# Optimization experiments

Hardware: AMD Instinct MI355X
Metric: run time of the kernel (lower is better)

The kernel has to match this reference:

```python
import jax, jax.numpy as jnp
import numpy as np

B, T, C, H = 2, 2048, 1024, 16  # batch, seq, n_embd, n_head


def setup_inputs() -> dict:
    key = jax.random.key(0)
    k1, k2, k3 = jax.random.split(key, 3)
    scale = 0.02
    return {
        "x": jax.random.normal(k1, (B, T, C), dtype=jnp.float32),
        "W_attn": jax.random.normal(k2, (3 * C, C), dtype=jnp.float32) * scale,
        "b_attn": jnp.zeros((3 * C,), dtype=jnp.float32),
        "W_proj": jax.random.normal(k3, (C, C), dtype=jnp.float32) * scale,
        "b_proj": jnp.zeros((C,), dtype=jnp.float32),
        "alpha": jnp.asarray(1.0, dtype=jnp.float32),
        "beta": jnp.asarray(0.1, dtype=jnp.float32),
        "gamma": jnp.asarray(0.1, dtype=jnp.float32),
    }


def reference(x, W_attn, b_attn, W_proj, b_proj, alpha, beta, gamma):
    Bx, Tx, Cx = x.shape
    d = Cx // H  # head dim
    qkv = x @ W_attn.T + b_attn                      # [B,T,3C]
    q, k, v = jnp.split(qkv, 3, axis=-1)

    def to_heads(t):
        return t.reshape(Bx, Tx, H, d).transpose(0, 2, 1, 3)  # [B,H,T,d]

    q, k, v = to_heads(q), to_heads(k), to_heads(v)

    inv_sqrt_d = jnp.asarray(1.0 / np.sqrt(d), dtype=x.dtype)
    scores = jnp.einsum('bhtd,bhsd->bhts', q, k) * inv_sqrt_d  # [B,H,T,T]

    causal = jnp.tril(jnp.ones((Tx, Tx), dtype=bool))
    scores = jnp.where(causal, scores, -jnp.inf)
    att = jax.nn.softmax(scores, axis=-1)

    # Id buffer = softmax(10000*eye) == identity; MC buffer = softmax(10000*tril)
    # == uniform causal prefix average: MC[i, j<=i] = 1/(i+1).
    id_m = jnp.eye(Tx, dtype=x.dtype)
    mc = causal.astype(x.dtype) / jnp.arange(1, Tx + 1, dtype=x.dtype)[:, None]

    shaped = beta * att + alpha * id_m - gamma * mc  # dropout p=0 -> identity
    y = jnp.einsum('bhts,bhsd->bhtd', shaped, v)     # [B,H,T,d]
    y = y.transpose(0, 2, 1, 3).reshape(Bx, Tx, Cx)
    return y @ W_proj.T + b_proj
```

## Files before the change

### kernel.cpp

```cpp
#include <hip/hip_runtime.h>
#include <stdint.h>

#define Bsz  2
#define Tseq 2048
#define Cemb 1024
#define NH   16
#define HD   64

typedef __attribute__((ext_vector_type(8))) __bf16 bf16x8;
typedef __attribute__((ext_vector_type(4))) float  f32x4;
typedef __attribute__((ext_vector_type(8))) unsigned short u16x8;

#define MFMA16(a, b, c) __builtin_amdgcn_mfma_f32_16x16x32_bf16((a), (b), (c), 0, 0, 0)

__device__ __forceinline__ unsigned short f2bf(float f) {
  union { float f; unsigned int u; } v; v.f = f;
  unsigned int u = v.u;
  u += 0x7fffu + ((u >> 16) & 1u);
  return (unsigned short)(u >> 16);
}
__device__ __forceinline__ float bf2f(unsigned short h) {
  union { unsigned int u; float f; } v; v.u = ((unsigned int)h) << 16;
  return v.f;
}
__device__ __forceinline__ unsigned int pack_bf2(float a, float b) {
  union { float f; unsigned int u; } va, vb; va.f = a; vb.f = b;
  return __builtin_amdgcn_perm(vb.u + 0x8000u, va.u + 0x8000u, 0x07060302u);
}

typedef __attribute__((address_space(1))) const unsigned int GU;
typedef __attribute__((address_space(3))) unsigned int LU;
__device__ __forceinline__ void load_lds16(const void* g, void* l) {
  __builtin_amdgcn_global_load_lds((GU*)g, (LU*)l, 16, 0, 0);
}

#define XE  4194304
#define WAE 3145728
__global__ void cast3_kernel(const float* __restrict__ x,
                             const float* __restrict__ wa,
                             const float* __restrict__ wp,
                             unsigned short* __restrict__ out) {
  const int i = (blockIdx.x * blockDim.x + threadIdx.x) * 4;
  const float* src;
  int off;
  if (i < XE) { src = x; off = i; }
  else if (i < XE + WAE) { src = wa; off = i - XE; }
  else { src = wp; off = i - (XE + WAE); }
  const float4 f = *(const float4*)(src + off);
  ushort4 o;
  o.x = f2bf(f.x); o.y = f2bf(f.y); o.z = f2bf(f.z); o.w = f2bf(f.w);
  *(ushort4*)(out + i) = o;
}

__global__ __launch_bounds__(256) void gemm_qkv_kernel(
    const unsigned short* __restrict__ A,
    const unsigned short* __restrict__ Bw,
    const float* __restrict__ bias,
    unsigned short* __restrict__ qkv,
    unsigned short* __restrict__ vt) {
  const int K = Cemb;
  __shared__ unsigned short sA[128 * 32];
  __shared__ unsigned short sB[128 * 32];
  const int tid = threadIdx.x;
  const int wave = tid >> 6, lane = tid & 63;
  const int quad = lane >> 4, lrow = lane & 15;
  const int l7 = lrow & 7;
  const int wm = (wave >> 1) * 64, wn = (wave & 1) * 64;
  const int tileM = blockIdx.y * 128, tileN = blockIdx.x * 128;

  f32x4 acc[4][4];
#pragma unroll
  for (int i = 0; i < 4; ++i)
#pragma unroll
    for (int j = 0; j < 4; ++j) acc[i][j] = (f32x4){0.f, 0.f, 0.f, 0.f};

  for (int k0 = 0; k0 < K; k0 += 32) {
    __syncthreads();
#pragma unroll
    for (int s = 0; s < 2; ++s) {
      const int cid = tid + s * 256;
      const int r = cid >> 2, ko = (cid & 3) * 8;
      load_lds16(&A[(size_t)(tileM + r) * K + k0 + ko], &sA[cid * 8]);
      load_lds16(&Bw[(size_t)(tileN + r) * K + k0 + ko], &sB[cid * 8]);
    }
    __syncthreads();
    bf16x8 af[4], bfm[4];
#pragma unroll
    for (int mt = 0; mt < 4; ++mt)
      af[mt] = *(const bf16x8*)&sA[(wm + mt * 16 + lrow) * 32 + quad * 8];
#pragma unroll
    for (int nt = 0; nt < 4; ++nt)
      bfm[nt] = *(const bf16x8*)&sB[(wn + nt * 16 + lrow) * 32 + quad * 8];
#pragma unroll
    for (int mt = 0; mt < 4; ++mt)
#pragma unroll
      for (int nt = 0; nt < 4; ++nt)
        acc[mt][nt] = MFMA16(af[mt], bfm[nt], acc[mt][nt]);
  }

  __syncthreads();
  unsigned short* sEp = sA + wave * 1024;
  float bias_v[4];
#pragma unroll
  for (int nt = 0; nt < 4; ++nt) bias_v[nt] = bias[tileN + wn + nt * 16 + lrow];
  const int gn0 = tileN + wn;
  const int part = gn0 >> 10, h = (gn0 & 1023) >> 6;
  const float qscl = (part == 0) ? 0.125f : 1.0f;

#pragma unroll
  for (int mt = 0; mt < 4; ++mt) {
#pragma unroll
    for (int nt = 0; nt < 4; ++nt)
#pragma unroll
      for (int reg = 0; reg < 4; ++reg) {
        const int q = quad * 4 + reg;
        const int ch = (nt * 2 + (lrow >> 3)) ^ (q & 7);
        sEp[q * 64 + ch * 8 + l7] = f2bf((acc[mt][nt][reg] + bias_v[nt]) * qscl);
      }
    __builtin_amdgcn_wave_barrier();
#pragma unroll
    for (int i = 0; i < 2; ++i) {
      const int c = i * 64 + lane;
      const int r = c >> 3, ch2 = c & 7;
      const u16x8 row = *(const u16x8*)&sEp[r * 64 + ((ch2 ^ (r & 7)) << 3)];
      const int gm = tileM + wm + mt * 16 + r;
      const int bb = gm >> 11, t = gm & 2047;
      *(u16x8*)&qkv[((((size_t)part * Bsz + bb) * NH + h) * Tseq + t) * HD + ch2 * 8] = row;
    }
    if (part == 2) {
      unsigned int w[8];
#pragma unroll
      for (int q = 0; q < 16; q += 2) {
        const unsigned short a0 =
            sEp[q * 64 + (((lane >> 3) ^ (q & 7)) << 3) + (lane & 7)];
        const unsigned short a1 =
            sEp[(q + 1) * 64 + (((lane >> 3) ^ ((q + 1) & 7)) << 3) + (lane & 7)];
        w[q >> 1] = (unsigned int)a0 | ((unsigned int)a1 << 16);
      }
      const int gm0 = tileM + wm + mt * 16;
      const int bb = gm0 >> 11, t0 = gm0 & 2047;
      unsigned short* dst = &vt[(((size_t)bb * NH + h) * HD + lane) * Tseq + t0];
      *(uint4*)(dst) = *(const uint4*)&w[0];
      *(uint4*)(dst + 8) = *(const uint4*)&w[4];
    }
    __builtin_amdgcn_wave_barrier();
  }
}

__global__ __launch_bounds__(256) void gemm_proj_kernel(
    const unsigned short* __restrict__ A,
    const unsigned short* __restrict__ Bw,
    const float* __restrict__ bias,
    float* __restrict__ out) {
  const int K = Cemb;
  __shared__ unsigned short sA[32 * 32];
  __shared__ unsigned short sB[128 * 32];
  const int tid = threadIdx.x;
  const int wave = tid >> 6, lane = tid & 63;
  const int quad = lane >> 4, lrow = lane & 15;
  const int wn = wave * 32;
  const int tileM = blockIdx.y * 32, tileN = blockIdx.x * 128;

  f32x4 acc[2][2];
#pragma unroll
  for (int i = 0; i < 2; ++i)
#pragma unroll
    for (int j = 0; j < 2; ++j) acc[i][j] = (f32x4){0.f, 0.f, 0.f, 0.f};

  for (int k0 = 0; k0 < K; k0 += 32) {
    __syncthreads();
    if (tid < 128) {
      const int r = tid >> 2, ko = (tid & 3) * 8;
      load_lds16(&A[(size_t)(tileM + r) * K + k0 + ko], &sA[tid * 8]);
    }
#pragma unroll
    for (int s = 0; s < 2; ++s) {
      const int cB = tid + s * 256;
      const int rB = cB >> 2, koB = (cB & 3) * 8;
      load_lds16(&Bw[(size_t)(tileN + rB) * K + k0 + koB], &sB[cB * 8]);
    }
    __syncthreads();
    bf16x8 af[2], bfm[2];
#pragma unroll
    for (int mt = 0; mt < 2; ++mt)
      af[mt] = *(const bf16x8*)&sA[(mt * 16 + lrow) * 32 + quad * 8];
#pragma unroll
    for (int nt = 0; nt < 2; ++nt)
      bfm[nt] = *(const bf16x8*)&sB[(wn + nt * 16 + lrow) * 32 + quad * 8];
#pragma unroll
    for (int mt = 0; mt < 2; ++mt)
#pragma unroll
      for (int nt = 0; nt < 2; ++nt)
        acc[mt][nt] = MFMA16(af[mt], bfm[nt], acc[mt][nt]);
  }

#pragma unroll
  for (int mt = 0; mt < 2; ++mt)
#pragma unroll
    for (int nt = 0; nt < 2; ++nt)
#pragma unroll
      for (int reg = 0; reg < 4; ++reg) {
        const int gm = tileM + mt * 16 + quad * 4 + reg;
        const int gn = tileN + wn + nt * 16 + lrow;
        out[(size_t)gm * Cemb + gn] = acc[mt][nt][reg] + bias[gn];
      }
}

__global__ __launch_bounds__(256) void attn_kernel(
    const unsigned short* __restrict__ qkv,
    const unsigned short* __restrict__ vt,
    const float* __restrict__ palpha, const float* __restrict__ pbeta,
    const float* __restrict__ pgamma,
    unsigned short* __restrict__ y) {
  __shared__ unsigned short sK[2][64 * 64];
  __shared__ unsigned short sVt[2][64 * 64];

  const int tid = threadIdx.x;
  const int wave = tid >> 6, lane = tid & 63;
  const int quad = lane >> 4, lrow = lane & 15;
  const int bh = blockIdx.y;
  const int b = bh >> 4, h = bh & 15;

  const size_t partStride = (size_t)Bsz * NH * Tseq * HD;
  const size_t headoff = (size_t)bh * Tseq * HD;
  const unsigned short* Q = qkv + headoff;
  const unsigned short* Kp = qkv + partStride + headoff;
  const unsigned short* Vp = qkv + 2 * partStride + headoff;
  const unsigned short* Vt_g = vt + (size_t)bh * HD * Tseq;

  const float alpha = palpha[0], beta = pbeta[0], gamma = pgamma[0];

  union { unsigned short u[8]; bf16x8 v; } onesU;
#pragma unroll
  for (int j = 0; j < 8; ++j) onesU.u[j] = 0x3F80;
  const bf16x8 onesF = onesU.v;

  const int qt = 31 - (int)blockIdx.x;
  const int q0 = qt * 64;

  const int qrow = q0 + wave * 16 + lrow;
  const bf16x8 bQ0 = *(const bf16x8*)&Q[(size_t)qrow * HD + quad * 8];
  const bf16x8 bQ1 = *(const bf16x8*)&Q[(size_t)qrow * HD + 32 + quad * 8];

  const int prow = ((lrow & 12) << 1) | (lrow & 3);

  f32x4 Ot[4], Ut[4], L;
#pragma unroll
  for (int dt = 0; dt < 4; ++dt) {
    Ot[dt] = (f32x4){0.f, 0.f, 0.f, 0.f};
    Ut[dt] = (f32x4){0.f, 0.f, 0.f, 0.f};
  }
  L = (f32x4){0.f, 0.f, 0.f, 0.f};

  auto stage_tile = [&](int it, int buf) {
    const int j0 = it * 64;
#pragma unroll
    for (int s = 0; s < 2; ++s) {
      const int c = tid + s * 256;
      const int r = c >> 3, cc = c & 7;
      const int pk = cc ^ (r & 7) ^ ((r & 16) >> 2);
      load_lds16(&Kp[(size_t)(j0 + r) * HD + pk * 8], &sK[buf][c * 8]);
      load_lds16(&Vt_g[(size_t)r * Tseq + j0 + pk * 8], &sVt[buf][c * 8]);
    }
  };

  stage_tile(0, 0);

  const int ntiles = qt + 1;
  for (int it = 0; it < ntiles; ++it) {
    const int cur = it & 1;
    __syncthreads();
    if (it + 1 < ntiles) stage_tile(it + 1, (it + 1) & 1);

    const unsigned short* K_ = sK[cur];
    const unsigned short* Vt_ = sVt[cur];
    const int j0 = it * 64;
    const bool diag = (it == qt);

    unsigned int pk2[4][2];
#pragma unroll
    for (int ct = 0; ct < 4; ++ct) {
      const int srow = (ct >> 1) * 32 + (ct & 1) * 4 + prow;
      const int hs = (srow & 7) ^ ((srow & 16) >> 2);
      const bf16x8 a0 = *(const bf16x8*)&K_[srow * 64 + ((quad ^ hs) << 3)];
      const bf16x8 a1 = *(const bf16x8*)&K_[srow * 64 + (((4 + quad) ^ hs) << 3)];
      f32x4 s = (f32x4){0.f, 0.f, 0.f, 0.f};
      s = MFMA16(a0, bQ0, s);
      s = MFMA16(a1, bQ1, s);
      float p[4];
      if (diag) {
        const int sbase = j0 + (ct >> 1) * 32 + (ct & 1) * 4 + quad * 8;
#pragma unroll
        for (int reg = 0; reg < 4; ++reg)
          p[reg] = __expf((sbase + reg > qrow) ? -1e30f : s[reg]);
      } else {
#pragma unroll
        for (int reg = 0; reg < 4; ++reg) p[reg] = __expf(s[reg]);
      }
      pk2[ct][0] = pack_bf2(p[0], p[1]);
      pk2[ct][1] = pack_bf2(p[2], p[3]);
    }
    union { unsigned int w[4]; bf16x8 v; } tu;
    tu.w[0] = pk2[0][0]; tu.w[1] = pk2[0][1]; tu.w[2] = pk2[1][0]; tu.w[3] = pk2[1][1];
    const bf16x8 P1 = tu.v;
    tu.w[0] = pk2[2][0]; tu.w[1] = pk2[2][1]; tu.w[2] = pk2[3][0]; tu.w[3] = pk2[3][1];
    const bf16x8 P2 = tu.v;

    L = MFMA16(onesF, P1, L);
    L = MFMA16(onesF, P2, L);

    bf16x8 u1 = onesF, u2 = onesF;
    if (diag) {
      union { unsigned short u[8]; bf16x8 v; } m0, m1;
#pragma unroll
      for (int jj = 0; jj < 8; ++jj) {
        m0.u[jj] = (j0 + quad * 8 + jj) <= qrow ? (unsigned short)0x3F80 : (unsigned short)0;
        m1.u[jj] = (j0 + 32 + quad * 8 + jj) <= qrow ? (unsigned short)0x3F80 : (unsigned short)0;
      }
      u1 = m0.v; u2 = m1.v;
    }

#pragma unroll
    for (int dt = 0; dt < 4; ++dt) {
      const int vr = dt * 16 + lrow;
      const int hvr = (vr & 7) ^ ((vr & 16) >> 2);
      const bf16x8 av0 = *(const bf16x8*)&Vt_[vr * 64 + ((quad ^ hvr) << 3)];
      const bf16x8 av1 = *(const bf16x8*)&Vt_[vr * 64 + (((4 + quad) ^ hvr) << 3)];
      Ot[dt] = MFMA16(av0, P1, Ot[dt]);
      Ot[dt] = MFMA16(av1, P2, Ot[dt]);
      Ut[dt] = MFMA16(av0, u1, Ut[dt]);
      Ut[dt] = MFMA16(av1, u2, Ut[dt]);
    }
  }

  const float bl = beta / L[0];
  const float gi = gamma / (float)(qrow + 1);
  const size_t ybase = ((size_t)b * Tseq + qrow) * Cemb + h * HD;
#pragma unroll
  for (int dt = 0; dt < 4; ++dt) {
    const int d0 = dt * 16 + quad * 4;
    const ushort4 vv4 = *(const ushort4*)&Vp[(size_t)qrow * HD + d0];
    const unsigned short vu[4] = {vv4.x, vv4.y, vv4.z, vv4.w};
    ushort4 o;
    unsigned short* op = (unsigned short*)&o;
#pragma unroll
    for (int reg = 0; reg < 4; ++reg) {
      const float yv = bl * Ot[dt][reg] + alpha * bf2f(vu[reg]) - gi * Ut[dt][reg];
      op[reg] = f2bf(yv);
    }
    *(ushort4*)&y[ybase + d0] = o;
  }
}

extern "C" void kernel_launch(void* const* d_in, const int* in_sizes, int n_in,
                              void* d_out, int out_size, void* d_ws, size_t ws_size,
                              hipStream_t stream) {
  const float* x  = (const float*)d_in[0];
  const float* Wa = (const float*)d_in[1];
  const float* ba = (const float*)d_in[2];
  const float* Wp = (const float*)d_in[3];
  const float* bp = (const float*)d_in[4];
  const float* alpha = (const float*)d_in[5];
  const float* beta  = (const float*)d_in[6];
  const float* gamma = (const float*)d_in[7];
  float* out = (float*)d_out;

  unsigned short* ws = (unsigned short*)d_ws;
  unsigned short* xb   = ws;
  unsigned short* wab  = xb + (size_t)XE;
  unsigned short* wpb  = wab + (size_t)WAE;
  unsigned short* qkvb = wpb + (size_t)1024 * 1024;
  unsigned short* yb   = qkvb + (size_t)3 * Bsz * NH * Tseq * HD;
  unsigned short* vtb  = yb + (size_t)Bsz * Tseq * Cemb;

  cast3_kernel<<<(XE + WAE + 1048576) / 4 / 256, 256, 0, stream>>>(x, Wa, Wp, xb);

  gemm_qkv_kernel<<<dim3(3072 / 128, 4096 / 128), 256, 0, stream>>>(xb, wab, ba, qkvb, vtb);
  attn_kernel<<<dim3(32, Bsz * NH), 256, 0, stream>>>(qkvb, vtb, alpha, beta, gamma, yb);
  gemm_proj_kernel<<<dim3(1024 / 128, 4096 / 32), 256, 0, stream>>>(yb, wpb, bp, out);
}
```

Measured before the change: 203.8 us.

## Load K and V tiles directly from global memory into registers, drop LDS staging

Removes the double-buffered LDS staging of K and V^T tiles and the per-iteration __syncthreads. Each wave now loads its K and V^T fragments straight from global memory into registers at the start of each tile. The launch bound gains a min-blocks hint of 4 to favour occupancy. This removes the barrier and LDS traffic, but each of the 4 waves reads the same K/V data from global/L2 separately, and the loads are no longer prefetched one tile ahead.

```diff
diff --git a/kernel.cpp b/kernel.cpp
--- a/kernel.cpp
+++ b/kernel.cpp
@@ -206,15 +206,12 @@
       }
 }
 
-__global__ __launch_bounds__(256) void attn_kernel(
+__global__ __launch_bounds__(256, 4) void attn_kernel(
     const unsigned short* __restrict__ qkv,
     const unsigned short* __restrict__ vt,
     const float* __restrict__ palpha, const float* __restrict__ pbeta,
     const float* __restrict__ pgamma,
     unsigned short* __restrict__ y) {
-  __shared__ unsigned short sK[2][64 * 64];
-  __shared__ unsigned short sVt[2][64 * 64];
-
   const int tid = threadIdx.x;
   const int wave = tid >> 6, lane = tid & 63;
   const int quad = lane >> 4, lrow = lane & 15;
@@ -252,41 +249,33 @@
   }
   L = (f32x4){0.f, 0.f, 0.f, 0.f};
 
-  auto stage_tile = [&](int it, int buf) {
-    const int j0 = it * 64;
-#pragma unroll
-    for (int s = 0; s < 2; ++s) {
-      const int c = tid + s * 256;
-      const int r = c >> 3, cc = c & 7;
-      const int pk = cc ^ (r & 7) ^ ((r & 16) >> 2);
-      load_lds16(&Kp[(size_t)(j0 + r) * HD + pk * 8], &sK[buf][c * 8]);
-      load_lds16(&Vt_g[(size_t)r * Tseq + j0 + pk * 8], &sVt[buf][c * 8]);
-    }
-  };
-
-  stage_tile(0, 0);
-
   const int ntiles = qt + 1;
   for (int it = 0; it < ntiles; ++it) {
-    const int cur = it & 1;
-    __syncthreads();
-    if (it + 1 < ntiles) stage_tile(it + 1, (it + 1) & 1);
-
-    const unsigned short* K_ = sK[cur];
-    const unsigned short* Vt_ = sVt[cur];
     const int j0 = it * 64;
     const bool diag = (it == qt);
 
-    unsigned int pk2[4][2];
+    bf16x8 a0[4], a1[4];
 #pragma unroll
     for (int ct = 0; ct < 4; ++ct) {
       const int srow = (ct >> 1) * 32 + (ct & 1) * 4 + prow;
-      const int hs = (srow & 7) ^ ((srow & 16) >> 2);
-      const bf16x8 a0 = *(const bf16x8*)&K_[srow * 64 + ((quad ^ hs) << 3)];
-      const bf16x8 a1 = *(const bf16x8*)&K_[srow * 64 + (((4 + quad) ^ hs) << 3)];
+      const unsigned short* kr = &Kp[(size_t)(j0 + srow) * HD];
+      a0[ct] = *(const bf16x8*)(kr + quad * 8);
+      a1[ct] = *(const bf16x8*)(kr + 32 + quad * 8);
+    }
+    bf16x8 av0[4], av1[4];
+#pragma unroll
+    for (int dt = 0; dt < 4; ++dt) {
+      const unsigned short* vrp = &Vt_g[(size_t)(dt * 16 + lrow) * Tseq + j0];
+      av0[dt] = *(const bf16x8*)(vrp + quad * 8);
+      av1[dt] = *(const bf16x8*)(vrp + 32 + quad * 8);
+    }
+
+    unsigned int pk2[4][2];
+#pragma unroll
+    for (int ct = 0; ct < 4; ++ct) {
       f32x4 s = (f32x4){0.f, 0.f, 0.f, 0.f};
-      s = MFMA16(a0, bQ0, s);
-      s = MFMA16(a1, bQ1, s);
+      s = MFMA16(a0[ct], bQ0, s);
+      s = MFMA16(a1[ct], bQ1, s);
       float p[4];
       if (diag) {
         const int sbase = j0 + (ct >> 1) * 32 + (ct & 1) * 4 + quad * 8;
@@ -322,14 +311,10 @@
 
 #pragma unroll
     for (int dt = 0; dt < 4; ++dt) {
-      const int vr = dt * 16 + lrow;
-      const int hvr = (vr & 7) ^ ((vr & 16) >> 2);
-      const bf16x8 av0 = *(const bf16x8*)&Vt_[vr * 64 + ((quad ^ hvr) << 3)];
-      const bf16x8 av1 = *(const bf16x8*)&Vt_[vr * 64 + (((4 + quad) ^ hvr) << 3)];
-      Ot[dt] = MFMA16(av0, P1, Ot[dt]);
-      Ot[dt] = MFMA16(av1, P2, Ot[dt]);
-      Ut[dt] = MFMA16(av0, u1, Ut[dt]);
-      Ut[dt] = MFMA16(av1, u2, Ut[dt]);
+      Ot[dt] = MFMA16(av0[dt], P1, Ot[dt]);
+      Ot[dt] = MFMA16(av1[dt], P2, Ot[dt]);
+      Ut[dt] = MFMA16(av0[dt], u1, Ut[dt]);
+      Ut[dt] = MFMA16(av1[dt], u2, Ut[dt]);
     }
   }
 
```

New measurement: 372.4 us. 1.83x slower.
